# Kernel tuning notes

Hardware: AMD Instinct MI355X
Metric: run time of the kernel (lower is better)

## Reference

```python
import jax, jax.numpy as jnp
import numpy as np

L = 32      # in_capsules
O = 32      # out_capsules
P = 16      # p_size
PD = 4      # p_dim = sqrt(p_size)
ETA = 1.0


def setup_inputs() -> dict:
    key = jax.random.key(0)
    k1, k2 = jax.random.split(key)
    # [B, H, W, L*16 + L]
    input_tensor = jax.random.normal(k1, (16, 14, 14, L * P + L), dtype=jnp.float32)
    # torch param: [1, K*K*L, O, 4, 4] with kernel_size=1
    weights = jax.random.normal(k2, (1, L, O, PD, PD), dtype=jnp.float32) * 0.25
    activation_bias = jnp.full((O,), 0.1, dtype=jnp.float32)
    return {"input_tensor": input_tensor, "weights": weights,
            "activation_bias": activation_bias}


def reference(input_tensor, weights, activation_bias):
    B = input_tensor.shape[0]
    # split poses / activations along channel dim
    poses_in = input_tensor[..., :-L].reshape(B, -1, PD, PD)   # [B, N, 4, 4], N = H*W*L
    acts_in = input_tensor[..., -L:].reshape(B, -1)            # [B, N]
    N = poses_in.shape[1]

    # share_transform: tile weights over spatial positions (H*W copies of the L blocks)
    w = jnp.tile(weights[0], (N // L, 1, 1, 1))                # [N, O, 4, 4]
    votes = jnp.einsum('bnij,nojk->bnoik', poses_in, w)        # [B, N, O, 4, 4]
    votes = votes.reshape(B, N, O, P)                          # [B, N, O, 16]

    # spectral routing
    votes = acts_in[:, :, None, None] * votes                  # weight by child activations
    votes = jnp.transpose(votes, (0, 2, 1, 3))                 # [B, O, N, 16]

    # top-1 right singular vector via eigendecomposition of the 16x16 gram matrix
    gram = jnp.einsum('bonp,bonq->bopq', votes, votes)         # [B, O, 16, 16]
    _, vecs = jnp.linalg.eigh(gram)                            # ascending eigenvalues
    poses = jax.lax.stop_gradient(vecs[..., -1])               # [B, O, 16] (detached, as in torch)

    yu = jnp.einsum('bonp,bop->bon', votes, poses)             # [B, O, N]
    yu_norm_sq = jnp.sum(yu * yu, axis=-1)                     # [B, O]
    y_fro_sq = jnp.sum(votes * votes, axis=(-1, -2))           # [B, O]
    activations = jax.nn.sigmoid(ETA * (yu_norm_sq / y_fro_sq - activation_bias))
    return activations, poses
```

## Files before the change

kernel.cpp:

```cpp
#include <hip/hip_runtime.h>
#include <hip/hip_bf16.h>


#define NSPAT 196

__device__ __forceinline__ float wsum64(float x) {
  x += __shfl_xor(x, 32);
  x += __shfl_xor(x, 16);
  x += __shfl_xor(x, 8);
  x += __shfl_xor(x, 4);
  x += __shfl_xor(x, 2);
  x += __shfl_xor(x, 1);
  return x;
}

__device__ __forceinline__ float rlanef(float x, int i) {
  return __int_as_float(__builtin_amdgcn_readlane(__float_as_int(x), i));
}

__global__ __launch_bounds__(256) void moments_kernel(const float* __restrict__ in,
                                                      float* __restrict__ Mout) {
  int b = blockIdx.x >> 5;
  int l = blockIdx.x & 31;
  __shared__ float ps[NSPAT][16];
  __shared__ float as2[NSPAT];
  int t = threadIdx.x;
  for (int j = t; j < NSPAT * 16; j += 256) {
    int s = j >> 4, p = j & 15;
    ps[s][p] = in[((size_t)(b * NSPAT + s)) * 544 + l * 16 + p];
  }
  for (int s = t; s < NSPAT; s += 256) {
    float a = in[((size_t)(b * NSPAT + s)) * 544 + 512 + l];
    as2[s] = a * a;
  }
  __syncthreads();
  int p = t >> 4, q = t & 15;
  float acc = 0.f;
  for (int s = 0; s < NSPAT; ++s) {
    acc += as2[s] * (ps[s][p] * ps[s][q]);
  }
  Mout[(size_t)blockIdx.x * 256 + t] = acc;
}

__global__ __launch_bounds__(256) void gram_kernel(const float* __restrict__ Min,
                                                   const float* __restrict__ W,
                                                   float* __restrict__ Gout) {
  int b = blockIdx.x >> 5;
  int o = blockIdx.x & 31;
  int t = threadIdx.x;
  __shared__ float Ms[32][256];
  __shared__ float Ws[32][16];
  for (int l = 0; l < 32; ++l)
    Ms[l][t] = Min[((size_t)(b * 32 + l)) * 256 + t];
  for (int j = t; j < 32 * 16; j += 256)
    Ws[j >> 4][j & 15] = W[((size_t)((j >> 4) * 32 + o)) * 16 + (j & 15)];
  __syncthreads();
  int p = t >> 4, q = t & 15;
  int i1 = p >> 2, k1 = p & 3, i2 = q >> 2, k2 = q & 3;
  float acc = 0.f;
  for (int l = 0; l < 32; ++l) {
    float sub = 0.f;
    for (int j2 = 0; j2 < 4; ++j2) {
      float inner = 0.f;
      for (int j = 0; j < 4; ++j)
        inner += Ws[l][j * 4 + k1] * Ms[l][(i1 * 4 + j) * 16 + (i2 * 4 + j2)];
      sub += Ws[l][j2 * 4 + k2] * inner;
    }
    acc += sub;
  }
  Gout[(size_t)blockIdx.x * 256 + t] = acc;
}

#define EPSF    5.9604645e-08f
#define EPS2F   (EPSF * EPSF)
#define SAFMINF 1.1754944e-38f

__device__ __forceinline__ float ssign(float a, float b) {
  return (b >= 0.f) ? fabsf(a) : -fabsf(a);
}

__device__ __forceinline__ float slapy2(float x, float y) {
  float xa = fabsf(x), ya = fabsf(y);
  float w = fmaxf(xa, ya), z = fminf(xa, ya);
  if (z == 0.f) return w;
  float t = z / w;
  return w * sqrtf(1.f + t * t);
}

__device__ __forceinline__ void slartg(float f, float g, float* c, float* s, float* r) {
  if (g == 0.f) {
    *c = 1.f; *s = 0.f; *r = f;
  } else if (f == 0.f) {
    *c = 0.f; *s = (g >= 0.f) ? 1.f : -1.f; *r = fabsf(g);
  } else {
    float d = sqrtf(f * f + g * g);
    *c = fabsf(f) / d;
    float rr = (f >= 0.f) ? d : -d;
    *s = g / rr;
    *r = rr;
  }
}

__device__ __forceinline__ void slaev2(float a, float b, float c,
                                       float* rt1, float* rt2, float* cs1, float* sn1) {
  float sm = a + c;
  float df = a - c;
  float adf = fabsf(df);
  float tb = b + b;
  float ab = fabsf(tb);
  float acmx, acmn;
  if (fabsf(a) > fabsf(c)) { acmx = a; acmn = c; } else { acmx = c; acmn = a; }
  float rt;
  if (adf > ab)      { float t = ab / adf; rt = adf * sqrtf(1.f + t * t); }
  else if (adf < ab) { float t = adf / ab; rt = ab * sqrtf(1.f + t * t); }
  else               { rt = ab * sqrtf(2.f); }
  int sgn1;
  if (sm < 0.f) {
    *rt1 = 0.5f * (sm - rt); sgn1 = -1;
    *rt2 = (acmx / *rt1) * acmn - (b / *rt1) * b;
  } else if (sm > 0.f) {
    *rt1 = 0.5f * (sm + rt); sgn1 = 1;
    *rt2 = (acmx / *rt1) * acmn - (b / *rt1) * b;
  } else {
    *rt1 = 0.5f * rt; *rt2 = -0.5f * rt; sgn1 = 1;
  }
  float cs; int sgn2;
  if (df >= 0.f) { cs = df + rt; sgn2 = 1; }
  else           { cs = df - rt; sgn2 = -1; }
  float acs = fabsf(cs);
  float c1, s1;
  if (acs > ab) {
    float ct = -tb / cs;
    s1 = 1.f / sqrtf(1.f + ct * ct);
    c1 = ct * s1;
  } else {
    if (ab == 0.f) { c1 = 1.f; s1 = 0.f; }
    else {
      float tn = -cs / tb;
      c1 = 1.f / sqrtf(1.f + tn * tn);
      s1 = tn * c1;
    }
  }
  if (sgn1 == sgn2) { float tn = c1; c1 = -s1; s1 = tn; }
  *cs1 = c1; *sn1 = s1;
}

__global__ __launch_bounds__(64) void eig_kernel(const float* __restrict__ G,
                                                 const float* __restrict__ bias,
                                                 float* __restrict__ out) {
  const int pid = blockIdx.x;
  const int lane = threadIdx.x;
  const int row = lane & 15;
  __shared__ float A[16][17];
  __shared__ float Zr[16][17];
  __shared__ float ddl[64][17];
  __shared__ float eel[64][17];
  __shared__ float ttl[64][17];

  for (int k = 0; k < 4; ++k) {
    int t = lane + 64 * k;
    int r = t >> 4, c = t & 15;
    int rr = r >= c ? r : c;
    int cc = r >= c ? c : r;
    A[r][c] = G[(size_t)pid * 256 + rr * 16 + cc];
    Zr[r][c] = (r == c) ? 1.f : 0.f;
  }
  float trc = (lane < 16) ? G[(size_t)pid * 256 + lane * 17] : 0.f;
  float trace = wsum64(trc);
  __syncthreads();

  for (int i = 0; i < 15; ++i) {
    float acol = (lane < 16) ? A[lane][i] : 0.f;
    float alpha = __shfl(acol, i + 1);
    float x = (lane >= i + 2 && lane < 16) ? acol : 0.f;
    float xns = wsum64(x * x);
    if (xns == 0.f) {
      eel[lane][i] = alpha;
      ttl[lane][i] = 0.f;
      continue;
    }
    float beta = (alpha >= 0.f ? -1.f : 1.f) * sqrtf(alpha * alpha + xns);
    float taui = (beta - alpha) / beta;
    float scal = 1.f / (alpha - beta);
    float vreg = 0.f;
    if (lane == i + 1) vreg = 1.f;
    else if (lane >= i + 2 && lane < 16) {
      vreg = acol * scal;
      A[lane][i] = vreg;
    }
    eel[lane][i] = beta;
    ttl[lane][i] = taui;
    float wr = 0.f;
    for (int cI = i + 1; cI < 16; ++cI) {
      float vc = __shfl(vreg, cI);
      if (lane >= i + 1 && lane < 16) wr += A[lane][cI] * vc;
    }
    wr *= taui;
    float dot = wsum64((lane >= i + 1 && lane < 16) ? wr * vreg : 0.f);
    float alpha2 = -0.5f * taui * dot;
    wr += alpha2 * vreg;
    for (int cI = i + 1; cI < 16; ++cI) {
      float wc = __shfl(wr, cI);
      float vc = __shfl(vreg, cI);
      if (lane >= i + 1 && lane < 16) A[lane][cI] -= vreg * wc + wr * vc;
    }
  }

  float di = (lane < 16) ? A[lane][lane] : 0.f;
  for (int j = 0; j < 16; ++j) ddl[lane][j] = __shfl(di, j);

  float* dd = ddl[lane];
  float* ee = eel[lane];
  ee[15] = 0.f;

  int m, l, lsv, lend, lendsv;
  int jtot = 0;
  const int nmaxit = 16 * 30;
  int l1 = 0;
  float dsn, esn;

outer:
  if (l1 > 15) goto done;
  if (l1 > 0) ee[l1 - 1] = 0.f;
  {
    int mm;
    for (mm = l1; mm < 15; ++mm) {
      float tst = fabsf(ee[mm]);
      if (tst == 0.f) break;
      if (tst <= (sqrtf(fabsf(dd[mm])) * sqrtf(fabsf(dd[mm + 1]))) * EPSF) {
        ee[mm] = 0.f;
        break;
      }
    }
    m = mm;
  }
  l = l1; lsv = l; lend = m; lendsv = lend;
  l1 = m + 1;
  if (lend == l) goto outer;
  {
    float an = 0.f;
    for (int k2 = l; k2 <= lend; ++k2) an = fmaxf(an, fabsf(dd[k2]));
    for (int k2 = l; k2 < lend; ++k2) an = fmaxf(an, fabsf(ee[k2]));
    if (an == 0.f) goto outer;
  }
  if (fabsf(dd[lend]) < fabsf(dd[l])) { lend = lsv; l = lendsv; }

  if (lend > l) {
ql_top:
    dsn = dd[row];
    esn = ee[row];
    {
      int mm;
      for (mm = l; mm < lend; ++mm) {
        float eI = rlanef(esn, mm);
        float tst = eI * eI;
        if (tst <= (EPS2F * fabsf(rlanef(dsn, mm))) * fabsf(rlanef(dsn, mm + 1)) + SAFMINF) break;
      }
      m = mm;
    }
    if (m < lend) ee[m] = 0.f;
    {
      float p = dd[l];
      if (m == l) {
        dd[l] = p;
        l = l + 1;
        if (l <= lend) goto ql_top;
        goto blk_done;
      }
      if (m == l + 1) {
        float rt1, rt2, c2, s2;
        slaev2(dd[l], ee[l], dd[l + 1], &rt1, &rt2, &c2, &s2);
        if (lane < 16) {
          float zj = Zr[lane][l], zj1 = Zr[lane][l + 1];
          Zr[lane][l]     = c2 * zj + s2 * zj1;
          Zr[lane][l + 1] = -s2 * zj + c2 * zj1;
        }
        dd[l] = rt1; dd[l + 1] = rt2; ee[l] = 0.f;
        l += 2;
        if (l <= lend) goto ql_top;
        goto blk_done;
      }
      if (jtot == nmaxit) goto blk_done;
      jtot++;
      float g = (rlanef(dsn, l + 1) - p) / (2.f * rlanef(esn, l));
      float r = slapy2(g, 1.f);
      g = rlanef(dsn, m) - p + rlanef(esn, l) / (g + ssign(r, g));
      float s = 1.f, c = 1.f;
      p = 0.f;
      for (int i = m - 1; i >= l; --i) {
        float eI = rlanef(esn, i);
        float f = s * eI;
        float bb = c * eI;
        slartg(g, f, &c, &s, &r);
        if (i != m - 1) ee[i + 1] = r;
        g = rlanef(dsn, i + 1) - p;
        r = (rlanef(dsn, i) - g) * s + 2.f * c * bb;
        p = s * r;
        dd[i + 1] = g + p;
        g = c * r - bb;
        if (lane < 16) {
          float zj = Zr[lane][i], zj1 = Zr[lane][i + 1];
          Zr[lane][i]     = c * zj - s * zj1;
          Zr[lane][i + 1] = s * zj + c * zj1;
        }
      }
      dd[l] -= p;
      ee[l] = g;
    }
    goto ql_top;
  } else {
qr_top:
    dsn = dd[row];
    esn = ee[row];
    {
      int mm;
      for (mm = l; mm > lend; --mm) {
        float eI = rlanef(esn, mm - 1);
        float tst = eI * eI;
        if (tst <= (EPS2F * fabsf(rlanef(dsn, mm))) * fabsf(rlanef(dsn, mm - 1)) + SAFMINF) break;
      }
      m = mm;
    }
    if (m > lend) ee[m - 1] = 0.f;
    {
      float p = dd[l];
      if (m == l) {
        dd[l] = p;
        l = l - 1;
        if (l >= lend) goto qr_top;
        goto blk_done;
      }
      if (m == l - 1) {
        float rt1, rt2, c2, s2;
        slaev2(dd[l - 1], ee[l - 1], dd[l], &rt1, &rt2, &c2, &s2);
        if (lane < 16) {
          float zj = Zr[lane][l - 1], zj1 = Zr[lane][l];
          Zr[lane][l - 1] = c2 * zj + s2 * zj1;
          Zr[lane][l]     = -s2 * zj + c2 * zj1;
        }
        dd[l - 1] = rt1; dd[l] = rt2; ee[l - 1] = 0.f;
        l -= 2;
        if (l >= lend) goto qr_top;
        goto blk_done;
      }
      if (jtot == nmaxit) goto blk_done;
      jtot++;
      float g = (rlanef(dsn, l - 1) - p) / (2.f * rlanef(esn, l - 1));
      float r = slapy2(g, 1.f);
      g = rlanef(dsn, m) - p + rlanef(esn, l - 1) / (g + ssign(r, g));
      float s = 1.f, c = 1.f;
      p = 0.f;
      for (int i = m; i <= l - 1; ++i) {
        float eI = rlanef(esn, i);
        float f = s * eI;
        float bb = c * eI;
        slartg(g, f, &c, &s, &r);
        if (i != m) ee[i - 1] = r;
        g = rlanef(dsn, i) - p;
        r = (rlanef(dsn, i + 1) - g) * s + 2.f * c * bb;
        p = s * r;
        dd[i] = g + p;
        g = c * r - bb;
        if (lane < 16) {
          float zj = Zr[lane][i], zj1 = Zr[lane][i + 1];
          Zr[lane][i]     = c * zj + s * zj1;
          Zr[lane][i + 1] = -s * zj + c * zj1;
        }
      }
      dd[l] -= p;
      ee[l - 1] = g;
    }
    goto qr_top;
  }
blk_done:
  goto outer;

done:;
  int kmax = 0;
  float dmax = dd[0];
  for (int j = 1; j < 16; ++j) {
    float dj = dd[j];
    if (dj > dmax) { dmax = dj; kmax = j; }
  }
  float vreg = (lane < 16) ? Zr[lane][kmax] : 0.f;
  for (int i = 14; i >= 0; --i) {
    float taui = ttl[lane][i];
    if (taui == 0.f) continue;
    float contrib;
    if (lane == i + 1) contrib = vreg;
    else if (lane >= i + 2 && lane < 16) contrib = A[lane][i] * vreg;
    else contrib = 0.f;
    float dot = wsum64(contrib);
    float td = taui * dot;
    if (lane == i + 1) vreg -= td;
    else if (lane >= i + 2 && lane < 16) vreg -= td * A[lane][i];
  }

  float act = 1.f / (1.f + expf(-(dmax / trace - bias[pid & 31])));
  if (lane == 0) out[pid] = act;
  if (lane < 16) out[512 + pid * 16 + lane] = vreg;
}

extern "C" void kernel_launch(void* const* d_in, const int* in_sizes, int n_in,
                              void* d_out, int out_size, void* d_ws, size_t ws_size,
                              hipStream_t stream) {
  const float* in   = (const float*)d_in[0];
  const float* W    = (const float*)d_in[1];
  const float* bias = (const float*)d_in[2];
  float* out = (float*)d_out;

  float* Mbuf = (float*)d_ws;
  float* Gbuf = Mbuf + 512 * 256;

  moments_kernel<<<512, 256, 0, stream>>>(in, Mbuf);
  gram_kernel<<<512, 256, 0, stream>>>(Mbuf, W, Gbuf);
  eig_kernel<<<512, 64, 0, stream>>>(Gbuf, bias, out);
}
```

Measured before the change: 259.0 us.

## Log Givens rotations and back-apply them to recover only the top eigenvector

Drops the full 16x16 eigenvector accumulation in LDS during the implicit QL/QR iterations. Each rotation's (c, s, index) is now logged to shared memory. After convergence the logged rotations are applied in reverse to the unit vector for the largest eigenvalue, using lane shuffles. Several diagonal and off-diagonal LDS reads are also replaced by readlane on register copies. The risks are that the backward pass is a serial chain of shuffles, and that results become silently wrong if more than 1024 rotations occur, since later entries are not logged.

```diff
diff --git a/kernel.cpp b/kernel.cpp
--- a/kernel.cpp
+++ b/kernel.cpp
@@ -145,6 +145,8 @@
   *cs1 = c1; *sn1 = s1;
 }
 
+#define MAXLOG 1024
+
 __global__ __launch_bounds__(64) void eig_kernel(const float* __restrict__ G,
                                                  const float* __restrict__ bias,
                                                  float* __restrict__ out) {
@@ -152,10 +154,11 @@
   const int lane = threadIdx.x;
   const int row = lane & 15;
   __shared__ float A[16][17];
-  __shared__ float Zr[16][17];
   __shared__ float ddl[64][17];
   __shared__ float eel[64][17];
   __shared__ float ttl[64][17];
+  __shared__ float2 logcs[MAXLOG];
+  __shared__ int    logi[MAXLOG];
 
   for (int k = 0; k < 4; ++k) {
     int t = lane + 64 * k;
@@ -163,7 +166,6 @@
     int rr = r >= c ? r : c;
     int cc = r >= c ? c : r;
     A[r][c] = G[(size_t)pid * 256 + rr * 16 + cc];
-    Zr[r][c] = (r == c) ? 1.f : 0.f;
   }
   float trc = (lane < 16) ? G[(size_t)pid * 256 + lane * 17] : 0.f;
   float trace = wsum64(trc);
@@ -217,17 +219,21 @@
   int jtot = 0;
   const int nmaxit = 16 * 30;
   int l1 = 0;
+  int nrot = 0;
   float dsn, esn;
 
 outer:
   if (l1 > 15) goto done;
   if (l1 > 0) ee[l1 - 1] = 0.f;
+  dsn = dd[row];
+  esn = ee[row];
   {
     int mm;
     for (mm = l1; mm < 15; ++mm) {
-      float tst = fabsf(ee[mm]);
+      float eI = rlanef(esn, mm);
+      float tst = fabsf(eI);
       if (tst == 0.f) break;
-      if (tst <= (sqrtf(fabsf(dd[mm])) * sqrtf(fabsf(dd[mm + 1]))) * EPSF) {
+      if (tst <= (sqrtf(fabsf(rlanef(dsn, mm))) * sqrtf(fabsf(rlanef(dsn, mm + 1)))) * EPSF) {
         ee[mm] = 0.f;
         break;
       }
@@ -239,11 +245,11 @@
   if (lend == l) goto outer;
   {
     float an = 0.f;
-    for (int k2 = l; k2 <= lend; ++k2) an = fmaxf(an, fabsf(dd[k2]));
-    for (int k2 = l; k2 < lend; ++k2) an = fmaxf(an, fabsf(ee[k2]));
+    for (int k2 = l; k2 <= lend; ++k2) an = fmaxf(an, fabsf(rlanef(dsn, k2)));
+    for (int k2 = l; k2 < lend; ++k2) an = fmaxf(an, fabsf(rlanef(esn, k2)));
     if (an == 0.f) goto outer;
   }
-  if (fabsf(dd[lend]) < fabsf(dd[l])) { lend = lsv; l = lendsv; }
+  if (fabsf(rlanef(dsn, lend)) < fabsf(rlanef(dsn, l))) { lend = lsv; l = lendsv; }
 
   if (lend > l) {
 ql_top:
@@ -260,7 +266,7 @@
     }
     if (m < lend) ee[m] = 0.f;
     {
-      float p = dd[l];
+      float p = rlanef(dsn, l);
       if (m == l) {
         dd[l] = p;
         l = l + 1;
@@ -269,12 +275,9 @@
       }
       if (m == l + 1) {
         float rt1, rt2, c2, s2;
-        slaev2(dd[l], ee[l], dd[l + 1], &rt1, &rt2, &c2, &s2);
-        if (lane < 16) {
-          float zj = Zr[lane][l], zj1 = Zr[lane][l + 1];
-          Zr[lane][l]     = c2 * zj + s2 * zj1;
-          Zr[lane][l + 1] = -s2 * zj + c2 * zj1;
-        }
+        slaev2(rlanef(dsn, l), rlanef(esn, l), rlanef(dsn, l + 1), &rt1, &rt2, &c2, &s2);
+        if (lane == 0 && nrot < MAXLOG) { logcs[nrot] = make_float2(c2, -s2); logi[nrot] = l; }
+        nrot++;
         dd[l] = rt1; dd[l + 1] = rt2; ee[l] = 0.f;
         l += 2;
         if (l <= lend) goto ql_top;
@@ -298,13 +301,10 @@
         p = s * r;
         dd[i + 1] = g + p;
         g = c * r - bb;
-        if (lane < 16) {
-          float zj = Zr[lane][i], zj1 = Zr[lane][i + 1];
-          Zr[lane][i]     = c * zj - s * zj1;
-          Zr[lane][i + 1] = s * zj + c * zj1;
-        }
-      }
-      dd[l] -= p;
+        if (lane == 0 && nrot < MAXLOG) { logcs[nrot] = make_float2(c, s); logi[nrot] = i; }
+        nrot++;
+      }
+      dd[l] = rlanef(dsn, l) - p;
       ee[l] = g;
     }
     goto ql_top;
@@ -323,7 +323,7 @@
     }
     if (m > lend) ee[m - 1] = 0.f;
     {
-      float p = dd[l];
+      float p = rlanef(dsn, l);
       if (m == l) {
         dd[l] = p;
         l = l - 1;
@@ -332,12 +332,9 @@
       }
       if (m == l - 1) {
         float rt1, rt2, c2, s2;
-        slaev2(dd[l - 1], ee[l - 1], dd[l], &rt1, &rt2, &c2, &s2);
-        if (lane < 16) {
-          float zj = Zr[lane][l - 1], zj1 = Zr[lane][l];
-          Zr[lane][l - 1] = c2 * zj + s2 * zj1;
-          Zr[lane][l]     = -s2 * zj + c2 * zj1;
-        }
+        slaev2(rlanef(dsn, l - 1), rlanef(esn, l - 1), rlanef(dsn, l), &rt1, &rt2, &c2, &s2);
+        if (lane == 0 && nrot < MAXLOG) { logcs[nrot] = make_float2(c2, -s2); logi[nrot] = l - 1; }
+        nrot++;
         dd[l - 1] = rt1; dd[l] = rt2; ee[l - 1] = 0.f;
         l -= 2;
         if (l >= lend) goto qr_top;
@@ -361,13 +358,10 @@
         p = s * r;
         dd[i] = g + p;
         g = c * r - bb;
-        if (lane < 16) {
-          float zj = Zr[lane][i], zj1 = Zr[lane][i + 1];
-          Zr[lane][i]     = c * zj + s * zj1;
-          Zr[lane][i + 1] = -s * zj + c * zj1;
-        }
-      }
-      dd[l] -= p;
+        if (lane == 0 && nrot < MAXLOG) { logcs[nrot] = make_float2(c, -s); logi[nrot] = i; }
+        nrot++;
+      }
+      dd[l] = rlanef(dsn, l) - p;
       ee[l - 1] = g;
     }
     goto qr_top;
@@ -376,13 +370,38 @@
   goto outer;
 
 done:;
+  dsn = dd[row];
   int kmax = 0;
-  float dmax = dd[0];
+  float dmax = rlanef(dsn, 0);
   for (int j = 1; j < 16; ++j) {
-    float dj = dd[j];
+    float dj = rlanef(dsn, j);
     if (dj > dmax) { dmax = dj; kmax = j; }
   }
-  float vreg = (lane < 16) ? Zr[lane][kmax] : 0.f;
+
+  float w = (lane == kmax) ? 1.f : 0.f;
+  {
+    int t = nrot - 1;
+    if (t > MAXLOG - 1) t = MAXLOG - 1;
+    while (t >= 0) {
+      int base = t & ~63;
+      float2 cs = logcs[base + lane];
+      int ii = logi[base + lane];
+      for (int k = t - base; k >= 0; --k) {
+        float c = rlanef(cs.x, k);
+        float sg = rlanef(cs.y, k);
+        int i = __builtin_amdgcn_readlane(ii, k);
+        float wup = __shfl_up(w, 1);
+        float wdn = __shfl_down(w, 1);
+        float nw = w;
+        if (lane == i) nw = c * w + sg * wdn;
+        else if (lane == i + 1) nw = -sg * wup + c * w;
+        w = nw;
+      }
+      t = base - 1;
+    }
+  }
+
+  float vreg = (lane < 16) ? w : 0.f;
   for (int i = 14; i >= 0; --i) {
     float taui = ttl[lane][i];
     if (taui == 0.f) continue;
```

New measurement: 257.0 us. Within noise of the previous version (-0.8%).
